# Kernel optimization log

Measured on AMD Instinct MI355X. Metric: run time of the kernel, lower is better.

The kernel has to match this reference:

```python
import jax, jax.numpy as jnp
import numpy as np

B, H, W = 8, 1024, 1280
EPS = 1e-7
MIN_DEPTH, MAX_DEPTH = 10.0, 255.0


def _constants(batch, view_to_syn='left'):
    trans = np.array([-4.14339018, -0.0238197036, -0.00190685259], np.float32)
    K_u = np.array([1035.30811, 0.0, 596.955017, 0.0, 1035.08765, 520.410034, 0.0, 0.0, 1.0], np.float32).reshape(3, 3)
    K_u[0, :] /= 1280.0
    K_u[1, :] /= 1024.0
    K_u4 = np.zeros((4, 4), np.float32); K_u4[:3, :3] = K_u; K_u4[3, 3] = 1.0
    K_d = np.array([1035.17419, 0.0, 688.361877, 0.0, 1034.979, 521.070801, 0.0, 0.0, 1.0], np.float32).reshape(3, 3)
    K_d[0, :] /= 1280.0
    K_d[1, :] /= 1024.0
    K_d4 = np.zeros((4, 4), np.float32); K_d4[:3, :3] = K_d; K_d4[3, 3] = 1.0
    if view_to_syn == 'right':
        src, tgt, t = K_u4, K_d4, trans
    else:
        src, tgt, t = K_d4, K_u4, -trans
    source_K = jnp.asarray(np.tile(src[None], (batch, 1, 1)))
    target_K = jnp.asarray(np.tile(tgt[None], (batch, 1, 1)))
    trans_vec = jnp.asarray(np.tile(t[None], (batch, 1)))
    return source_K, target_K, trans_vec


def setup_inputs() -> dict:
    key = jax.random.key(0)
    k1, k2 = jax.random.split(key)
    img = jax.random.normal(k1, (B, 3, H, W), jnp.float32)
    pred_disp = jax.random.uniform(k2, (B, 1, H, W), jnp.float32)
    source_K, target_K, trans_vec = _constants(B, 'left')
    return {"img": img, "pred_disp": pred_disp, "source_K": source_K,
            "target_K": target_K, "trans_vec": trans_vec}


def _grid_sample_border(img, grid):
    """Bilinear grid_sample, padding_mode='border', align_corners=False (torch default).
    img: [B,C,H,W], grid: [B,H,W,2] in [-1,1] (x,y). Returns [B,C,H,W]."""
    b, c, h, w = img.shape
    x = (grid[..., 0] + 1.0) * w * 0.5 - 0.5  # [B,H,W]
    y = (grid[..., 1] + 1.0) * h * 0.5 - 0.5
    x0f = jnp.floor(x); y0f = jnp.floor(y)
    wx = (x - x0f)[:, None]  # [B,1,H,W]
    wy = (y - y0f)[:, None]
    x0 = jnp.clip(x0f.astype(jnp.int32), 0, w - 1)
    x1 = jnp.clip(x0f.astype(jnp.int32) + 1, 0, w - 1)
    y0 = jnp.clip(y0f.astype(jnp.int32), 0, h - 1)
    y1 = jnp.clip(y0f.astype(jnp.int32) + 1, 0, h - 1)
    gather = jax.vmap(lambda im, yi, xi: im[:, yi, xi])  # -> [B,C,H,W]
    i00 = gather(img, y0, x0)
    i01 = gather(img, y0, x1)
    i10 = gather(img, y1, x0)
    i11 = gather(img, y1, x1)
    return (i00 * (1 - wx) * (1 - wy) + i01 * wx * (1 - wy)
            + i10 * (1 - wx) * wy + i11 * wx * wy)


def reference(img, pred_disp, source_K, target_K, trans_vec):
    b, _, h, w = img.shape
    # disp -> depth
    min_disp, max_disp = 1.0 / MAX_DEPTH, 1.0 / MIN_DEPTH
    scaled_disp = min_disp + (max_disp - min_disp) * pred_disp
    depth = 1.0 / scaled_disp  # [B,1,H,W]
    # homogeneous pixel grid [3, H*W]
    xs, ys = jnp.meshgrid(jnp.arange(w, dtype=jnp.float32),
                          jnp.arange(h, dtype=jnp.float32), indexing='xy')
    pix = jnp.stack([xs.reshape(-1), ys.reshape(-1), jnp.ones(h * w, jnp.float32)], 0)
    # backproject
    inv_K = jnp.linalg.inv(source_K)[:, :3, :3]  # [B,3,3]
    cam = jnp.einsum('bij,jn->bin', inv_K, pix) * depth.reshape(b, 1, -1)  # [B,3,HW]
    cam4 = jnp.concatenate([cam, jnp.ones((b, 1, h * w), cam.dtype)], axis=1)  # [B,4,HW]
    # extrinsic: R = I, so T @ R = translation matrix
    T = jnp.tile(jnp.eye(4, dtype=img.dtype)[None], (b, 1, 1)).at[:, :3, 3].set(trans_vec.reshape(b, 3))
    P = jnp.matmul(target_K, T)[:, :3, :]  # [B,3,4]
    cp = jnp.matmul(P, cam4)  # [B,3,HW]
    pc = cp[:, :2] / (cp[:, 2:3] + EPS)  # [B,2,HW]
    pc = pc.reshape(b, 2, h, w).transpose(0, 2, 3, 1)  # [B,H,W,2]
    scale = jnp.array([w - 1, h - 1], dtype=pc.dtype)
    grid = (pc / scale - 0.5) * 2.0
    return _grid_sample_border(img, grid)
```

## Files before the change

### kernel.cpp

```cpp
#include <hip/hip_runtime.h>

#define BB 8
#define HH 1024
#define WW 1280
#define HW (HH * WW)
#define EPSF 1e-7f

typedef float f2u __attribute__((ext_vector_type(2), aligned(4)));

__device__ __forceinline__ float fast_rcp(float x) {
    float r = __builtin_amdgcn_rcpf(x);
    r = r * __builtin_fmaf(-x, r, 2.0f);
    return r;
}

__global__ void precompute_consts(
    const float* __restrict__ srcK, const float* __restrict__ tgtK,
    const float* __restrict__ trans, float* __restrict__ cb)
{
    const int b = threadIdx.x;
    if (b >= BB) return;
    const float* sK = srcK + b * 16;
    const float* tK = tgtK + b * 16;
    const float* tv = trans + b * 3;

    const float fsx = sK[0], csx = sK[2];
    const float fsy = sK[5], csy = sK[6];
    const float ftx = tK[0], ctx = tK[2];
    const float fty = tK[5], cty = tK[6];
    const float t0 = tv[0], t1 = tv[1], t2 = tv[2];

    const float Sx = (float)WW / (float)(WW - 1);
    const float Sy = (float)HH / (float)(HH - 1);
    const float rfsx = 1.0f / fsx;
    const float rfsy = 1.0f / fsy;
    float* c = cb + b * 8;
    c[0] = ftx * rfsx * Sx;
    c[1] = __builtin_fmaf(-ftx * csx, rfsx, ctx) * Sx;
    c[2] = (ftx * t0 + ctx * t2) * Sx;
    c[3] = fty * rfsy * Sy;
    c[4] = __builtin_fmaf(-fty * csy, rfsy, cty) * Sy;
    c[5] = (fty * t1 + cty * t2) * Sy;
    c[6] = t2 + EPSF;
    c[7] = 0.0f;
}

__global__ __launch_bounds__(256) void synth_view_kernel(
    const float* __restrict__ img, const float* __restrict__ disp,
    const float* __restrict__ cbuf, float* __restrict__ out)
{
    const int x = blockIdx.x * 256 + threadIdx.x;
    const int y = blockIdx.y;
    const int b = blockIdx.z;

    const float* cb = cbuf + b * 8;
    const float A00 = cb[0], A02 = cb[1], C0 = cb[2];
    const float A11 = cb[3], A12 = cb[4], C1 = cb[5];
    const float t2e = cb[6];

    const int rowoff = y * WW + x;
    const float dsp = __builtin_nontemporal_load(disp + b * HW + rowoff);

    const float mind = 1.0f / 255.0f;
    const float rng  = 0.1f - mind;
    const float sd   = __builtin_fmaf(dsp, rng, mind);
    const float r    = fast_rcp(__builtin_fmaf(t2e, sd, 1.0f));

    const float ax = __builtin_fmaf(A00, (float)x, A02);
    const float ay = __builtin_fmaf(A11, (float)y, A12);
    const float sx = __builtin_fmaf(__builtin_fmaf(C0, sd, ax), r, -0.5f);
    const float sy = __builtin_fmaf(__builtin_fmaf(C1, sd, ay), r, -0.5f);

    const int ix = (int)floorf(sx);
    const int iy = (int)floorf(sy);
    const int ixc = min(max(ix, 0), WW - 2);
    const int iyc = min(max(iy, 0), HH - 2);
    const float wx = fminf(fmaxf(sx - (float)ixc, 0.0f), 1.0f);
    const float wy = fminf(fmaxf(sy - (float)iyc, 0.0f), 1.0f);

    const int o0 = iyc * WW + ixc;
    const int o1 = o0 + WW;

    const float wxm = 1.0f - wx, wym = 1.0f - wy;
    const float w00 = wxm * wym, w01 = wx * wym;
    const float w10 = wxm * wy,  w11 = wx * wy;

    const float* imb  = img + b * (3 * HW);
    float*       outb = out + b * (3 * HW) + rowoff;

#pragma unroll
    for (int c = 0; c < 3; ++c) {
        const float* ic = imb + c * HW;
        const f2u v0 = *reinterpret_cast<const f2u*>(ic + o0);
        const f2u v1 = *reinterpret_cast<const f2u*>(ic + o1);
        float acc =          v0.x * w00;
        acc = __builtin_fmaf(v0.y, w01, acc);
        acc = __builtin_fmaf(v1.x, w10, acc);
        acc = __builtin_fmaf(v1.y, w11, acc);
        __builtin_nontemporal_store(acc, outb + c * HW);
    }
}

extern "C" void kernel_launch(void* const* d_in, const int* in_sizes, int n_in,
                              void* d_out, int out_size, void* d_ws, size_t ws_size,
                              hipStream_t stream) {
    const float* img   = (const float*)d_in[0];
    const float* disp  = (const float*)d_in[1];
    const float* srcK  = (const float*)d_in[2];
    const float* tgtK  = (const float*)d_in[3];
    const float* trans = (const float*)d_in[4];
    float* out = (float*)d_out;
    float* cb  = (float*)d_ws;

    precompute_consts<<<dim3(1), dim3(64), 0, stream>>>(srcK, tgtK, trans, cb);

    dim3 block(256, 1, 1);
    dim3 grid(WW / 256, HH, BB);
    synth_view_kernel<<<grid, block, 0, stream>>>(img, disp, cb, out);
}
```

Before: 256.6 us.

## Stage image tiles in LDS and process 16 rows per thread

Each block now loads an 18x264 halo window per channel into LDS with 16-byte vector loads. Each thread then handles 16 output rows of one column, reading its bilinear taps from LDS instead of doing scattered global loads. The grid is flattened and remapped so that neighbouring blocks cover vertically adjacent tiles. Sample coordinates are clamped to the window, which relies on the warp shift staying within a few pixels for the given intrinsics and disparity range. The roughly 56 KB of LDS per block limits occupancy.

```diff
diff --git a/kernel.cpp b/kernel.cpp
--- a/kernel.cpp
+++ b/kernel.cpp
@@ -6,7 +6,14 @@
 #define HW (HH * WW)
 #define EPSF 1e-7f
 
-typedef float f2u __attribute__((ext_vector_type(2), aligned(4)));
+#define TH 16
+#define TCOLS 264
+#define SROWS 18
+#define CPR 66
+#define CHUNKS (3 * SROWS * CPR)
+#define CH_PAD 3584
+
+typedef float f4 __attribute__((ext_vector_type(4)));
 
 __device__ __forceinline__ float fast_rcp(float x) {
     float r = __builtin_amdgcn_rcpf(x);
@@ -49,55 +56,90 @@
     const float* __restrict__ img, const float* __restrict__ disp,
     const float* __restrict__ cbuf, float* __restrict__ out)
 {
-    const int x = blockIdx.x * 256 + threadIdx.x;
-    const int y = blockIdx.y;
-    const int b = blockIdx.z;
+    __shared__ __align__(16) float st[CH_PAD * 4];
+
+    const int tid = threadIdx.x;
+    const int wid = blockIdx.x;
+    const int r   = wid & 7;
+    int q = wid >> 3;
+    const int tyl = q & 7;  q >>= 3;
+    const int xb  = q % 5;
+    const int b   = q / 5;
+    const int y0  = (r * 8 + tyl) * TH;
+    const int x0  = xb * 256;
+    const int x   = x0 + tid;
+
+    const float* imb = img + (size_t)b * 3 * HW;
+
+    float dsp[TH];
+#pragma unroll
+    for (int j = 0; j < TH; ++j)
+        dsp[j] = __builtin_nontemporal_load(
+            disp + (size_t)b * HW + (size_t)(y0 + j) * WW + x);
+
+    f4 v[14];
+#pragma unroll
+    for (int i = 0; i < 14; ++i) {
+        const int qq = i * 256 + tid;
+        const int qc = min(qq, CHUNKS - 1);
+        const int c  = qc / (SROWS * CPR);
+        const int rm = qc - c * (SROWS * CPR);
+        const int ri = rm / CPR;
+        const int k  = rm - ri * CPR;
+        const int row = min(max(y0 - 1 + ri, 0), HH - 1);
+        const int col = min(max(x0 - 4 + 4 * k, 0), WW - 4);
+        v[i] = *reinterpret_cast<const f4*>(imb + (size_t)(c * HH + row) * WW + col);
+    }
+#pragma unroll
+    for (int i = 0; i < 14; ++i) {
+        const int qq = i * 256 + tid;
+        *reinterpret_cast<f4*>(&st[qq * 4]) = v[i];
+    }
 
     const float* cb = cbuf + b * 8;
     const float A00 = cb[0], A02 = cb[1], C0 = cb[2];
     const float A11 = cb[3], A12 = cb[4], C1 = cb[5];
     const float t2e = cb[6];
 
-    const int rowoff = y * WW + x;
-    const float dsp = __builtin_nontemporal_load(disp + b * HW + rowoff);
-
     const float mind = 1.0f / 255.0f;
     const float rng  = 0.1f - mind;
-    const float sd   = __builtin_fmaf(dsp, rng, mind);
-    const float r    = fast_rcp(__builtin_fmaf(t2e, sd, 1.0f));
+    const float axc  = __builtin_fmaf(A00, (float)x, A02);
 
-    const float ax = __builtin_fmaf(A00, (float)x, A02);
-    const float ay = __builtin_fmaf(A11, (float)y, A12);
-    const float sx = __builtin_fmaf(__builtin_fmaf(C0, sd, ax), r, -0.5f);
-    const float sy = __builtin_fmaf(__builtin_fmaf(C1, sd, ay), r, -0.5f);
+    __syncthreads();
 
-    const int ix = (int)floorf(sx);
-    const int iy = (int)floorf(sy);
-    const int ixc = min(max(ix, 0), WW - 2);
-    const int iyc = min(max(iy, 0), HH - 2);
-    const float wx = fminf(fmaxf(sx - (float)ixc, 0.0f), 1.0f);
-    const float wy = fminf(fmaxf(sy - (float)iyc, 0.0f), 1.0f);
-
-    const int o0 = iyc * WW + ixc;
-    const int o1 = o0 + WW;
-
-    const float wxm = 1.0f - wx, wym = 1.0f - wy;
-    const float w00 = wxm * wym, w01 = wx * wym;
-    const float w10 = wxm * wy,  w11 = wx * wy;
-
-    const float* imb  = img + b * (3 * HW);
-    float*       outb = out + b * (3 * HW) + rowoff;
+    float* outb = out + (size_t)b * 3 * HW + x;
 
 #pragma unroll
-    for (int c = 0; c < 3; ++c) {
-        const float* ic = imb + c * HW;
-        const f2u v0 = *reinterpret_cast<const f2u*>(ic + o0);
-        const f2u v1 = *reinterpret_cast<const f2u*>(ic + o1);
-        float acc =          v0.x * w00;
-        acc = __builtin_fmaf(v0.y, w01, acc);
-        acc = __builtin_fmaf(v1.x, w10, acc);
-        acc = __builtin_fmaf(v1.y, w11, acc);
-        __builtin_nontemporal_store(acc, outb + c * HW);
+    for (int j = 0; j < TH; ++j) {
+        const int y = y0 + j;
+        const float sd  = __builtin_fmaf(dsp[j], rng, mind);
+        const float rrz = fast_rcp(__builtin_fmaf(t2e, sd, 1.0f));
+        const float ayc = __builtin_fmaf(A11, (float)y, A12);
+        const float sx  = __builtin_fmaf(__builtin_fmaf(C0, sd, axc), rrz, -0.5f);
+        const float sy  = __builtin_fmaf(__builtin_fmaf(C1, sd, ayc), rrz, -0.5f);
+
+        const int ixc = min(max((int)floorf(sx), 0), WW - 2);
+        const int iyc = min(max((int)floorf(sy), 0), HH - 2);
+        const float wx = fminf(fmaxf(sx - (float)ixc, 0.0f), 1.0f);
+        const float wy = fminf(fmaxf(sy - (float)iyc, 0.0f), 1.0f);
+
+        const int wcol = min(max(ixc - x0 + 4, 0), TCOLS - 2);
+        const int wrow = min(max(iyc - y0 + 1, 0), SROWS - 2);
+
+        const float wxm = 1.0f - wx, wym = 1.0f - wy;
+        const float w00 = wxm * wym, w01 = wx * wym;
+        const float w10 = wxm * wy,  w11 = wx * wy;
+
+        const int base = wrow * TCOLS + wcol;
+#pragma unroll
+        for (int c = 0; c < 3; ++c) {
+            const float* p = &st[(c * SROWS) * TCOLS + base];
+            float acc =          p[0]         * w00;
+            acc = __builtin_fmaf(p[1],         w01, acc);
+            acc = __builtin_fmaf(p[TCOLS],     w10, acc);
+            acc = __builtin_fmaf(p[TCOLS + 1], w11, acc);
+            __builtin_nontemporal_store(acc, outb + (size_t)c * HW + (size_t)y * WW);
+        }
     }
 }
 
@@ -115,6 +157,6 @@
     precompute_consts<<<dim3(1), dim3(64), 0, stream>>>(srcK, tgtK, trans, cb);
 
     dim3 block(256, 1, 1);
-    dim3 grid(WW / 256, HH, BB);
+    dim3 grid(5 * 64 * BB, 1, 1);
     synth_view_kernel<<<grid, block, 0, stream>>>(img, disp, cb, out);
 }
```

Result: faster. 249.4 us (-2.8%).
